# Kernel optimization log

Measured on AMD Instinct MI355X. Metric: run time of the kernel, lower is better.

The kernel has to match this reference:

```python
import jax, jax.numpy as jnp
import numpy as np

N = 50000      # nodes
E = 800000     # edges
HID = 64       # hidden_dim
HEADS = 4
DH = HID // HEADS
PIN = 128      # person_in_dim
DIN = 64       # disease_in_dim
NEXP = 4       # num_experts
K = 2          # topk
L = 2          # n_layers
NEG = 0.2      # gat_neg_slope


def setup_inputs() -> dict:
    key = jax.random.key(0)
    ks = iter(jax.random.split(key, 64))
    nrm = lambda shp, s=0.05: jax.random.normal(next(ks), shp, jnp.float32) * s
    d = {}
    d["features"] = jax.random.normal(next(ks), (N, PIN), jnp.float32)
    d["node_types"] = jax.random.randint(next(ks), (N,), 0, 2)
    d["src"] = jax.random.randint(next(ks), (E,), 0, N)
    d["dst"] = jax.random.randint(next(ks), (E,), 0, N)
    d["W_person"] = nrm((PIN, HID)); d["b_person"] = jnp.zeros((HID,), jnp.float32)
    d["W_disease"] = nrm((DIN, HID)); d["b_disease"] = jnp.zeros((HID,), jnp.float32)
    d["gat_W"] = nrm((L, HID, HID)); d["gat_al"] = nrm((L, HEADS, DH)); d["gat_ar"] = nrm((L, HEADS, DH))
    d["gin_eps"] = jnp.zeros((L,), jnp.float32)
    d["gin_W1"] = nrm((L, HID, HID)); d["gin_b1"] = jnp.zeros((L, HID), jnp.float32)
    d["gin_W2"] = nrm((L, HID, HID)); d["gin_b2"] = jnp.zeros((L, HID), jnp.float32)
    for p in ("gat", "gin"):
        d[p + "_gW"] = nrm((HID, NEXP)); d[p + "_gb"] = jnp.zeros((NEXP,), jnp.float32)
        d[p + "_eW1"] = nrm((NEXP, HID, HID // 2)); d[p + "_eb1"] = jnp.zeros((NEXP, HID // 2), jnp.float32)
        d[p + "_eW2"] = nrm((NEXP, HID // 2, HID)); d[p + "_eb2"] = jnp.zeros((NEXP, HID), jnp.float32)
    d["fg_W1"] = nrm((2 * HID, HID)); d["fg_b1"] = jnp.zeros((HID,), jnp.float32)
    d["fg_W2"] = nrm((HID, HID)); d["fg_b2"] = jnp.zeros((HID,), jnp.float32)
    return d


def _edge_softmax(logits, dst):
    m = jax.ops.segment_max(logits, dst, num_segments=N)
    e = jnp.exp(logits - m[dst])
    s = jax.ops.segment_sum(e, dst, num_segments=N)
    return e / (s[dst] + 1e-9)


def _gat(h, src, dst, gat_W, gat_al, gat_ar):
    for l in range(L):
        hW = (h @ gat_W[l]).reshape(N, HEADS, DH)
        el = (hW * gat_al[l]).sum(-1)                    # [N, HEADS]
        er = (hW * gat_ar[l]).sum(-1)
        lg = jax.nn.leaky_relu(el[src] + er[dst], NEG)   # [E, HEADS]
        a = _edge_softmax(lg, dst)
        out = jax.ops.segment_sum(hW[src] * a[:, :, None], dst, num_segments=N)
        h2 = out.reshape(N, HID) + h                     # residual=True
        h = jax.nn.relu(h2) if l < L - 1 else h2
    return h


def _gin(h, src, dst, gin_eps, gin_W1, gin_b1, gin_W2, gin_b2):
    deg = jax.ops.segment_sum(jnp.ones((E,), jnp.float32), dst, num_segments=N)
    inv = 1.0 / jnp.maximum(deg, 1.0)
    for l in range(L):
        agg = jax.ops.segment_sum(h[src], dst, num_segments=N) * inv[:, None]  # 'mean' aggregator
        x = (1.0 + gin_eps[l]) * h + agg                 # learn_eps=True
        x = jax.nn.relu(x @ gin_W1[l] + gin_b1[l]) @ gin_W2[l] + gin_b2[l]     # 2-layer MLP
        h = jax.nn.relu(x) if l < L - 1 else x
    return h


def _expert(h, gW, gb, eW1, eb1, eW2, eb2):
    probs = jax.nn.softmax(h @ gW + gb, axis=-1)         # [N, NEXP]
    topv, topi = jax.lax.top_k(probs, K)
    topv = topv / topv.sum(-1, keepdims=True)
    hot = jax.nn.one_hot(topi, NEXP, dtype=h.dtype)      # [N, K, NEXP]
    w = (hot * topv[..., None]).sum(1)                   # [N, NEXP] sparse weights
    e1 = jax.nn.relu(jnp.einsum('nd,edh->neh', h, eW1) + eb1)
    e2 = jnp.einsum('neh,ehd->ned', e1, eW2) + eb2       # [N, NEXP, HID]
    out = (e2 * w[:, :, None]).sum(1)
    f = hot.sum(1).mean(0)                               # routed fraction per expert
    P = probs.mean(0)
    aux = NEXP * jnp.sum(f * P)                          # switch-style load balancing
    return out, aux


def reference(features, node_types, src, dst, W_person, b_person, W_disease, b_disease,
              gat_W, gat_al, gat_ar, gin_eps, gin_W1, gin_b1, gin_W2, gin_b2,
              gat_gW, gat_gb, gat_eW1, gat_eb1, gat_eW2, gat_eb2,
              gin_gW, gin_gb, gin_eW1, gin_eb1, gin_eW2, gin_eb2,
              fg_W1, fg_b1, fg_W2, fg_b2):
    # per-type projection + scatter into shared buffer
    hp = features[:, :PIN] @ W_person + b_person
    hd = features[:, :DIN] @ W_disease + b_disease
    h = jnp.where((node_types == 0)[:, None], hp, hd)
    z_gat = _gat(h, src, dst, gat_W, gat_al, gat_ar)
    z_gin = _gin(h, src, dst, gin_eps, gin_W1, gin_b1, gin_W2, gin_b2)
    zg, aux_g = _expert(z_gat, gat_gW, gat_gb, gat_eW1, gat_eb1, gat_eW2, gat_eb2)
    zi, aux_i = _expert(z_gin, gin_gW, gin_gb, gin_eW1, gin_eb1, gin_eW2, gin_eb2)
    z = zi * zg
    u = jnp.concatenate([zg, zi], axis=-1)
    gate = jax.nn.sigmoid(jax.nn.relu(u @ fg_W1 + fg_b1) @ fg_W2 + fg_b2)
    u_prime = gate  # source calls fusion_gate(u) twice -> identical deterministic value
    z = gate * z + (1.0 - gate) * u_prime
    return z, aux_i + aux_g
```

## Files before the change

### kernel.cpp

```cpp
#include <hip/hip_runtime.h>

#define NN 50000
#define EE 800000
#define NEG 0.2f
#define NBLK_SCAN 196
#define NBG 391
#define NBE 196
#define RBLK 782
#define NBKT 98
#define BCAP 9216
#define EPB 2048
#define NBINA 391

typedef __attribute__((ext_vector_type(8))) short s8;
typedef __attribute__((ext_vector_type(4))) float f4;

__device__ __forceinline__ float leaky(float x) { return x > 0.f ? x : NEG * x; }
__device__ __forceinline__ unsigned bf16r(float x) {
    unsigned u = __float_as_uint(x);
    return (u + 0x7fffu + ((u >> 16) & 1u)) >> 16;
}
__device__ __forceinline__ float lo16(unsigned p) { return __uint_as_float(p << 16); }
__device__ __forceinline__ float hi16(unsigned p) { return __uint_as_float(p & 0xffff0000u); }

__device__ __forceinline__ s8 a_from_f32(const float* p) {
    float4 u = *reinterpret_cast<const float4*>(p);
    float4 v = *reinterpret_cast<const float4*>(p + 4);
    s8 r;
    r[0] = (short)bf16r(u.x); r[1] = (short)bf16r(u.y);
    r[2] = (short)bf16r(u.z); r[3] = (short)bf16r(u.w);
    r[4] = (short)bf16r(v.x); r[5] = (short)bf16r(v.y);
    r[6] = (short)bf16r(v.z); r[7] = (short)bf16r(v.w);
    return r;
}

__global__ __launch_bounds__(256) void k_binA(const int* __restrict__ src,
        const int* __restrict__ dst, int* __restrict__ degcnt,
        int* __restrict__ bktcnt, unsigned* __restrict__ bkt) {
    __shared__ int cnt[NBKT];
    __shared__ int base[NBKT];
    for (int i = threadIdx.x; i < NBKT; i += 256) cnt[i] = 0;
    __syncthreads();
    int e0 = blockIdx.x * EPB;
    int d[8], s[8];
    #pragma unroll
    for (int i = 0; i < 8; i++) {
        int e = e0 + i * 256 + threadIdx.x;
        if (e < EE) {
            d[i] = dst[e]; s[i] = src[e];
            atomicAdd(&degcnt[d[i]], 1);
            atomicAdd(&cnt[d[i] >> 9], 1);
        } else d[i] = -1;
    }
    __syncthreads();
    for (int i = threadIdx.x; i < NBKT; i += 256)
        base[i] = atomicAdd(&bktcnt[i], cnt[i]);
    __syncthreads();
    for (int i = threadIdx.x; i < NBKT; i += 256) cnt[i] = 0;
    __syncthreads();
    #pragma unroll
    for (int i = 0; i < 8; i++) {
        if (d[i] >= 0) {
            int b = d[i] >> 9;
            int p = base[b] + atomicAdd(&cnt[b], 1);
            if (p < BCAP)
                bkt[(size_t)b * BCAP + p] = ((unsigned)s[i] << 9) | (unsigned)(d[i] & 511);
        }
    }
}

__global__ void k_scan_a(const int* __restrict__ degcnt, int* __restrict__ bsums) {
    __shared__ int sm[4];
    int i = blockIdx.x * 256 + threadIdx.x;
    int v = (i < NN) ? degcnt[i] : 0;
    #pragma unroll
    for (int o = 1; o < 64; o <<= 1) v += __shfl_xor(v, o, 64);
    if ((threadIdx.x & 63) == 0) sm[threadIdx.x >> 6] = v;
    __syncthreads();
    if (threadIdx.x == 0) bsums[blockIdx.x] = sm[0] + sm[1] + sm[2] + sm[3];
}

__global__ void k_scan_b(const int* __restrict__ bsums, int* __restrict__ bpre) {
    __shared__ int sm[256];
    int t = threadIdx.x;
    sm[t] = (t < NBLK_SCAN) ? bsums[t] : 0;
    __syncthreads();
    for (int off = 1; off < 256; off <<= 1) {
        int u = (t >= off) ? sm[t - off] : 0;
        __syncthreads();
        sm[t] += u;
        __syncthreads();
    }
    if (t < NBLK_SCAN) bpre[t] = (t == 0) ? 0 : sm[t - 1];
}

__global__ void k_scan_c(const int* __restrict__ degcnt, const int* __restrict__ bpre,
                         int* __restrict__ row_start) {
    __shared__ int sm[256];
    int t = threadIdx.x;
    int i = blockIdx.x * 256 + t;
    int v = (i < NN) ? degcnt[i] : 0;
    sm[t] = v;
    __syncthreads();
    for (int off = 1; off < 256; off <<= 1) {
        int u = (t >= off) ? sm[t - off] : 0;
        __syncthreads();
        sm[t] += u;
        __syncthreads();
    }
    int incl = sm[t];
    if (i < NN) row_start[i] = bpre[blockIdx.x] + incl - v;
    if (i == NN - 1) row_start[NN] = bpre[blockIdx.x] + incl;
}

__global__ __launch_bounds__(256) void k_binB_pre(
        const int* __restrict__ row_start, const int* __restrict__ bktcnt,
        const unsigned* __restrict__ bkt, int* __restrict__ csr_src,
        const float* __restrict__ feat, const int* __restrict__ types,
        const float* __restrict__ Wp, const float* __restrict__ bp,
        const float* __restrict__ Wd, const float* __restrict__ bd,
        const float* __restrict__ gW, const float* __restrict__ al,
        const float* __restrict__ ar,
        float* __restrict__ h0f, unsigned* __restrict__ P,
        float* __restrict__ el, float* __restrict__ er) {
    __shared__ unsigned short WpT[64 * 136];
    __shared__ unsigned short WdT[64 * 72];
    __shared__ unsigned short WgT[64 * 72];
    __shared__ unsigned short y0s[4][16 * 72];
    __shared__ int kur[512];
    if (blockIdx.x < NBKT) {
        int b = blockIdx.x;
        int d0 = b << 9;
        for (int i = threadIdx.x; i < 512; i += 256) {
            int d = d0 + i;
            kur[i] = (d < NN) ? row_start[d] : 0;
        }
        __syncthreads();
        int cnt = bktcnt[b]; if (cnt > BCAP) cnt = BCAP;
        for (int i = threadIdx.x; i < cnt; i += 256) {
            unsigned v = bkt[(size_t)b * BCAP + i];
            int p = atomicAdd(&kur[v & 511], 1);
            csr_src[p] = (int)(v >> 9);
        }
        return;
    }
    for (int idx = threadIdx.x; idx < 128 * 64; idx += 256) {
        int k = idx >> 6, n = idx & 63;
        WpT[n * 136 + k] = (unsigned short)bf16r(Wp[idx]);
    }
    for (int idx = threadIdx.x; idx < 64 * 64; idx += 256) {
        int k = idx >> 6, n = idx & 63;
        WdT[n * 72 + k] = (unsigned short)bf16r(Wd[idx]);
        WgT[n * 72 + k] = (unsigned short)bf16r(gW[idx]);
    }
    __syncthreads();
    int wv = threadIdx.x >> 6, lane = threadIdx.x & 63;
    int quad = lane >> 4, l16 = lane & 15;
    int gw2 = (blockIdx.x - NBKT) * 4 + wv;
    int mtEnd = gw2 * 2 + 2; if (mtEnd > 3125) mtEnd = 3125;
    for (int mt = gw2 * 2; mt < mtEnd; mt++) {
        int row0 = mt * 16;
        const float* arow = feat + (size_t)(row0 + l16) * 128;
        f4 accp[4], accd[4];
        #pragma unroll
        for (int t = 0; t < 4; t++) { accp[t] = f4{0.f,0.f,0.f,0.f}; accd[t] = f4{0.f,0.f,0.f,0.f}; }
        #pragma unroll
        for (int ks = 0; ks < 4; ks++) {
            s8 a = a_from_f32(arow + ks * 32 + quad * 8);
            #pragma unroll
            for (int t = 0; t < 4; t++) {
                s8 b = *(const s8*)&WpT[(t * 16 + l16) * 136 + ks * 32 + quad * 8];
                accp[t] = __builtin_amdgcn_mfma_f32_16x16x32_bf16(a, b, accp[t], 0, 0, 0);
                if (ks < 2) {
                    s8 bd_ = *(const s8*)&WdT[(t * 16 + l16) * 72 + ks * 32 + quad * 8];
                    accd[t] = __builtin_amdgcn_mfma_f32_16x16x32_bf16(a, bd_, accd[t], 0, 0, 0);
                }
            }
        }
        int ty[4];
        #pragma unroll
        for (int r = 0; r < 4; r++) ty[r] = types[row0 + quad * 4 + r];
        float vv[4][4];
        #pragma unroll
        for (int t = 0; t < 4; t++) {
            int col = t * 16 + l16;
            float bpv = bp[col], bdv = bd[col];
            #pragma unroll
            for (int r = 0; r < 4; r++) {
                float v = ty[r] ? (accd[t][r] + bdv) : (accp[t][r] + bpv);
                vv[t][r] = v;
                h0f[(size_t)(row0 + quad * 4 + r) * 64 + col] = v;
                y0s[wv][(quad * 4 + r) * 72 + col] = (unsigned short)bf16r(v);
            }
        }
        s8 a0 = *(const s8*)&y0s[wv][l16 * 72 + quad * 8];
        s8 a1 = *(const s8*)&y0s[wv][l16 * 72 + 32 + quad * 8];
        f4 hw[4];
        #pragma unroll
        for (int t = 0; t < 4; t++) {
            hw[t] = f4{0.f,0.f,0.f,0.f};
            s8 b0 = *(const s8*)&WgT[(t * 16 + l16) * 72 + quad * 8];
            hw[t] = __builtin_amdgcn_mfma_f32_16x16x32_bf16(a0, b0, hw[t], 0, 0, 0);
            s8 b1_ = *(const s8*)&WgT[(t * 16 + l16) * 72 + 32 + quad * 8];
            hw[t] = __builtin_amdgcn_mfma_f32_16x16x32_bf16(a1, b1_, hw[t], 0, 0, 0);
        }
        #pragma unroll
        for (int t = 0; t < 4; t++) {
            int col = t * 16 + l16;
            float alv = al[col], arv = ar[col];
            #pragma unroll
            for (int r = 0; r < 4; r++) {
                int row = row0 + quad * 4 + r;
                float h = hw[t][r];
                P[(size_t)row * 64 + col] = bf16r(h) | (bf16r(vv[t][r]) << 16);
                float pl = h * alv, pr = h * arv;
                #pragma unroll
                for (int m = 1; m < 16; m <<= 1) {
                    pl += __shfl_xor(pl, m, 64);
                    pr += __shfl_xor(pr, m, 64);
                }
                if (l16 == 0) {
                    el[(size_t)row * 4 + t] = pl;
                    er[(size_t)row * 4 + t] = pr;
                }
            }
        }
    }
}

template <int RELU>
__global__ void k_edges(const int* __restrict__ rows, const int* __restrict__ csr,
                        const unsigned* __restrict__ Pin,
                        const float* __restrict__ el, const float* __restrict__ er,
                        const float* __restrict__ gat_in, const float* __restrict__ gin_in,
                        const float* __restrict__ eps_p,
                        float* __restrict__ vgf, unsigned short* __restrict__ vgb,
                        unsigned short* __restrict__ xb) {
    __shared__ float ews[4][256];
    int wv = threadIdx.x >> 6, lane = threadIdx.x & 63;
    int n = blockIdx.x * 4 + wv;
    int st = rows[n], dg = rows[n + 1] - st;
    int hd = lane >> 4;
    float4 erv = *reinterpret_cast<const float4*>(er + (size_t)n * 4);
    float accg = 0.f, acci = 0.f, ssum = 0.f;
    for (int base = 0; base < dg; base += 64) {
        int rem = dg - base; if (rem > 64) rem = 64;
        int myi = 0;
        if (lane < rem) {
            myi = csr[st + base + lane];
            float4 lv = *reinterpret_cast<const float4*>(el + (size_t)myi * 4);
            float4 ev;
            ev.x = __expf(leaky(lv.x + erv.x));
            ev.y = __expf(leaky(lv.y + erv.y));
            ev.z = __expf(leaky(lv.z + erv.z));
            ev.w = __expf(leaky(lv.w + erv.w));
            *reinterpret_cast<float4*>(&ews[wv][lane * 4]) = ev;
        }
        int j = 0;
        for (; j + 4 <= rem; j += 4) {
            int s0 = __shfl(myi, j, 64),     s1 = __shfl(myi, j + 1, 64);
            int s2 = __shfl(myi, j + 2, 64), s3 = __shfl(myi, j + 3, 64);
            unsigned p0 = Pin[(size_t)s0 * 64 + lane];
            unsigned p1 = Pin[(size_t)s1 * 64 + lane];
            unsigned p2 = Pin[(size_t)s2 * 64 + lane];
            unsigned p3 = Pin[(size_t)s3 * 64 + lane];
            float a0 = ews[wv][(j + 0) * 4 + hd];
            float a1 = ews[wv][(j + 1) * 4 + hd];
            float a2 = ews[wv][(j + 2) * 4 + hd];
            float a3 = ews[wv][(j + 3) * 4 + hd];
            accg += a0 * lo16(p0) + a1 * lo16(p1) + a2 * lo16(p2) + a3 * lo16(p3);
            acci += hi16(p0) + hi16(p1) + hi16(p2) + hi16(p3);
            ssum += a0 + a1 + a2 + a3;
        }
        for (; j < rem; j++) {
            int s0 = __shfl(myi, j, 64);
            unsigned p0 = Pin[(size_t)s0 * 64 + lane];
            float a0 = ews[wv][j * 4 + hd];
            accg += a0 * lo16(p0); acci += hi16(p0); ssum += a0;
        }
    }
    float vg = accg / (ssum + 1e-9f) + gat_in[(size_t)n * 64 + lane];
    if (RELU) vg = fmaxf(vg, 0.f);
    float invd = 1.0f / fmaxf((float)dg, 1.0f);
    float x = (1.0f + eps_p[0]) * gin_in[(size_t)n * 64 + lane] + acci * invd;
    size_t off = (size_t)n * 64 + lane;
    vgf[off] = vg;
    vgb[off] = (unsigned short)bf16r(vg);
    xb[off] = (unsigned short)bf16r(x);
}

template <int L>
__global__ __launch_bounds__(256) void k_mlp(const unsigned short* __restrict__ Gx,
        const unsigned short* __restrict__ Eb,
        const float* __restrict__ W1, const float* __restrict__ b1,
        const float* __restrict__ W2, const float* __restrict__ b2,
        const float* __restrict__ gatW, const float* __restrict__ al,
        const float* __restrict__ ar,
        unsigned short* __restrict__ Fb, float* __restrict__ Cf,
        unsigned* __restrict__ P, float* __restrict__ el, float* __restrict__ er) {
    __shared__ unsigned short W1T[64 * 72];
    __shared__ unsigned short W2T[64 * 72];
    __shared__ unsigned short WgT[(L == 0) ? 64 * 72 : 64];
    __shared__ unsigned short y1s[4][16 * 72];
    for (int idx = threadIdx.x; idx < 64 * 64; idx += 256) {
        int k = idx >> 6, n = idx & 63;
        W1T[n * 72 + k] = (unsigned short)bf16r(W1[idx]);
        W2T[n * 72 + k] = (unsigned short)bf16r(W2[idx]);
        if (L == 0) WgT[n * 72 + k] = (unsigned short)bf16r(gatW[idx]);
    }
    __syncthreads();
    int wv = threadIdx.x >> 6, lane = threadIdx.x & 63;
    int quad = lane >> 4, l16 = lane & 15;
    int gw = blockIdx.x * 4 + wv;
    int mtEnd = gw * 2 + 2; if (mtEnd > 3125) mtEnd = 3125;
    for (int mt = gw * 2; mt < mtEnd; mt++) {
        int row0 = mt * 16;
        const unsigned short* arow = Gx + (size_t)(row0 + l16) * 64;
        s8 a0 = *(const s8*)(arow + quad * 8);
        s8 a1 = *(const s8*)(arow + 32 + quad * 8);
        f4 acc1[4];
        #pragma unroll
        for (int t = 0; t < 4; t++) {
            acc1[t] = f4{0.f,0.f,0.f,0.f};
            s8 b0 = *(const s8*)&W1T[(t * 16 + l16) * 72 + quad * 8];
            acc1[t] = __builtin_amdgcn_mfma_f32_16x16x32_bf16(a0, b0, acc1[t], 0, 0, 0);
            s8 b1_ = *(const s8*)&W1T[(t * 16 + l16) * 72 + 32 + quad * 8];
            acc1[t] = __builtin_amdgcn_mfma_f32_16x16x32_bf16(a1, b1_, acc1[t], 0, 0, 0);
        }
        #pragma unroll
        for (int t = 0; t < 4; t++) {
            float b1v = b1[t * 16 + l16];
            #pragma unroll
            for (int r = 0; r < 4; r++) {
                float v = fmaxf(acc1[t][r] + b1v, 0.f);
                y1s[wv][(quad * 4 + r) * 72 + t * 16 + l16] = (unsigned short)bf16r(v);
            }
        }
        s8 c0 = *(const s8*)&y1s[wv][l16 * 72 + quad * 8];
        s8 c1 = *(const s8*)&y1s[wv][l16 * 72 + 32 + quad * 8];
        f4 acc2[4];
        #pragma unroll
        for (int t = 0; t < 4; t++) {
            acc2[t] = f4{0.f,0.f,0.f,0.f};
            s8 b0 = *(const s8*)&W2T[(t * 16 + l16) * 72 + quad * 8];
            acc2[t] = __builtin_amdgcn_mfma_f32_16x16x32_bf16(c0, b0, acc2[t], 0, 0, 0);
            s8 b1_ = *(const s8*)&W2T[(t * 16 + l16) * 72 + 32 + quad * 8];
            acc2[t] = __builtin_amdgcn_mfma_f32_16x16x32_bf16(c1, b1_, acc2[t], 0, 0, 0);
        }
        unsigned short vb[4][4];
        #pragma unroll
        for (int t = 0; t < 4; t++) {
            int col = t * 16 + l16;
            float b2v = b2[col];
            #pragma unroll
            for (int r = 0; r < 4; r++) {
                float v = acc2[t][r] + b2v;
                if (L == 0) v = fmaxf(v, 0.f);
                size_t off = (size_t)(row0 + quad * 4 + r) * 64 + col;
                unsigned short vb16 = (unsigned short)bf16r(v);
                vb[t][r] = vb16;
                Fb[off] = vb16;
                Cf[off] = v;
            }
        }
        if (L == 0) {
            const unsigned short* erow = Eb + (size_t)(row0 + l16) * 64;
            s8 e0 = *(const s8*)(erow + quad * 8);
            s8 e1 = *(const s8*)(erow + 32 + quad * 8);
            f4 hw[4];
            #pragma unroll
            for (int t = 0; t < 4; t++) {
                hw[t] = f4{0.f,0.f,0.f,0.f};
                s8 b0 = *(const s8*)&WgT[(t * 16 + l16) * 72 + quad * 8];
                hw[t] = __builtin_amdgcn_mfma_f32_16x16x32_bf16(e0, b0, hw[t], 0, 0, 0);
                s8 b1_ = *(const s8*)&WgT[(t * 16 + l16) * 72 + 32 + quad * 8];
                hw[t] = __builtin_amdgcn_mfma_f32_16x16x32_bf16(e1, b1_, hw[t], 0, 0, 0);
            }
            #pragma unroll
            for (int t = 0; t < 4; t++) {
                int col = t * 16 + l16;
                float alv = al[col], arv = ar[col];
                #pragma unroll
                for (int r = 0; r < 4; r++) {
                    int row = row0 + quad * 4 + r;
                    float h = hw[t][r];
                    P[(size_t)row * 64 + col] = bf16r(h) | ((unsigned)vb[t][r] << 16);
                    float pl = h * alv, pr = h * arv;
                    #pragma unroll
                    for (int m = 1; m < 16; m <<= 1) {
                        pl += __shfl_xor(pl, m, 64);
                        pr += __shfl_xor(pr, m, 64);
                    }
                    if (l16 == 0) {
                        el[(size_t)row * 4 + t] = pl;
                        er[(size_t)row * 4 + t] = pr;
                    }
                }
            }
        }
    }
}

__global__ __launch_bounds__(256) void k_route(const float* __restrict__ zg,
        const float* __restrict__ zi,
        const float* __restrict__ ggW, const float* __restrict__ ggb,
        const float* __restrict__ igW, const float* __restrict__ igb,
        float* __restrict__ wgtg, float* __restrict__ wgti,
        float* __restrict__ stats) {
    __shared__ float zs[64][65];
    __shared__ float gws[256];
    __shared__ float sstat[16];
    if (threadIdx.x < 16) sstat[threadIdx.x] = 0.f;
    int n0 = blockIdx.x * 64;
    int wv = threadIdx.x >> 6, lane = threadIdx.x & 63;
    for (int q = 0; q < 2; q++) {
        const float* Z = q ? zi : zg;
        const float* GW = q ? igW : ggW;
        const float* GB = q ? igb : ggb;
        gws[threadIdx.x] = GW[threadIdx.x];
        #pragma unroll
        for (int r = 0; r < 16; r++) {
            int row = wv * 16 + r;
            int n = n0 + row;
            zs[row][lane] = (n < NN) ? Z[(size_t)n * 64 + lane] : 0.f;
        }
        __syncthreads();
        int node = threadIdx.x >> 2, e = threadIdx.x & 3;
        float lg = GB[e];
        #pragma unroll 8
        for (int k = 0; k < 64; k++) lg += zs[node][k] * gws[k * 4 + e];
        float b = __shfl_xor(lg, 1, 64);
        float c = __shfl_xor(lg, 2, 64);
        float d = __shfl_xor(b, 2, 64);
        float arr[4];
        arr[e] = lg; arr[e ^ 1] = b; arr[e ^ 2] = c; arr[e ^ 3] = d;
        int n = n0 + node;
        if (e == 0 && n < NN) {
            float mx = fmaxf(fmaxf(arr[0], arr[1]), fmaxf(arr[2], arr[3]));
            float ex0 = __expf(arr[0] - mx), ex1 = __expf(arr[1] - mx);
            float ex2 = __expf(arr[2] - mx), ex3 = __expf(arr[3] - mx);
            float inv = 1.0f / (ex0 + ex1 + ex2 + ex3);
            float pr[4] = {ex0 * inv, ex1 * inv, ex2 * inv, ex3 * inv};
            int i1 = 0; float v1 = pr[0];
            #pragma unroll
            for (int t = 1; t < 4; t++) if (pr[t] > v1) { v1 = pr[t]; i1 = t; }
            int i2 = -1; float v2 = -1.f;
            #pragma unroll
            for (int t = 0; t < 4; t++) if (t != i1 && pr[t] > v2) { v2 = pr[t]; i2 = t; }
            float wsum = v1 + v2;
            float wq[4] = {0.f, 0.f, 0.f, 0.f};
            wq[i1] = v1 / wsum; wq[i2] = v2 / wsum;
            float* WD = q ? wgti : wgtg;
            *reinterpret_cast<float4*>(WD + (size_t)n * 4) = float4{wq[0], wq[1], wq[2], wq[3]};
            #pragma unroll
            for (int t = 0; t < 4; t++) atomicAdd(&sstat[q * 8 + t], pr[t]);
            atomicAdd(&sstat[q * 8 + 4 + i1], 1.f);
            atomicAdd(&sstat[q * 8 + 4 + i2], 1.f);
        }
        __syncthreads();
    }
    if (threadIdx.x < 16) atomicAdd(&stats[threadIdx.x], sstat[threadIdx.x]);
}

__global__ __launch_bounds__(256) void k_expert(const unsigned short* __restrict__ Eb,
        const unsigned short* __restrict__ Fb,
        const float* __restrict__ g_eW1, const float* __restrict__ g_eb1,
        const float* __restrict__ g_eW2, const float* __restrict__ g_eb2,
        const float* __restrict__ i_eW1, const float* __restrict__ i_eb1,
        const float* __restrict__ i_eW2, const float* __restrict__ i_eb2,
        const float* __restrict__ wgtg, const float* __restrict__ wgti,
        float* __restrict__ moegf, float* __restrict__ moeif,
        unsigned short* __restrict__ ub) {
    __shared__ unsigned short w1t[4 * 32 * 72];
    __shared__ unsigned short w2t[4 * 64 * 40];
    __shared__ unsigned short y1s[4][16 * 40];
    int p = (blockIdx.x >= NBE) ? 1 : 0;
    int bb = blockIdx.x - p * NBE;
    const unsigned short* Ab = p ? Fb : Eb;
    const float* eW1 = p ? i_eW1 : g_eW1;
    const float* eb1 = p ? i_eb1 : g_eb1;
    const float* eW2 = p ? i_eW2 : g_eW2;
    const float* eb2 = p ? i_eb2 : g_eb2;
    const float* wgt = p ? wgti : wgtg;
    float* moef = p ? moeif : moegf;
    int qoff = p ? 64 : 0;
    for (int g = threadIdx.x; g < 8192; g += 256) {
        int e = g >> 11, rem = g & 2047;
        int k = rem >> 5, n = rem & 31;
        w1t[e * 2304 + n * 72 + k] = (unsigned short)bf16r(eW1[g]);
    }
    for (int g = threadIdx.x; g < 8192; g += 256) {
        int e = g >> 11, rem = g & 2047;
        int k = rem >> 6, n = rem & 63;
        w2t[e * 2560 + n * 40 + k] = (unsigned short)bf16r(eW2[g]);
    }
    __syncthreads();
    int wv = threadIdx.x >> 6, lane = threadIdx.x & 63;
    int quad = lane >> 4, l16 = lane & 15;
    int gw = bb * 4 + wv;
    int mtEnd = gw * 4 + 4; if (mtEnd > 3125) mtEnd = 3125;
    for (int mt = gw * 4; mt < mtEnd; mt++) {
        int row0 = mt * 16;
        const unsigned short* arow = Ab + (size_t)(row0 + l16) * 64;
        s8 a0 = *(const s8*)(arow + quad * 8);
        s8 a1 = *(const s8*)(arow + 32 + quad * 8);
        f4 outacc[4];
        #pragma unroll
        for (int t = 0; t < 4; t++) outacc[t] = f4{0.f,0.f,0.f,0.f};
        for (int e = 0; e < 4; e++) {
            f4 acc1[2];
            #pragma unroll
            for (int t = 0; t < 2; t++) {
                acc1[t] = f4{0.f,0.f,0.f,0.f};
                s8 b0 = *(const s8*)&w1t[e * 2304 + (t * 16 + l16) * 72 + quad * 8];
                acc1[t] = __builtin_amdgcn_mfma_f32_16x16x32_bf16(a0, b0, acc1[t], 0, 0, 0);
                s8 b1_ = *(const s8*)&w1t[e * 2304 + (t * 16 + l16) * 72 + 32 + quad * 8];
                acc1[t] = __builtin_amdgcn_mfma_f32_16x16x32_bf16(a1, b1_, acc1[t], 0, 0, 0);
            }
            #pragma unroll
            for (int t = 0; t < 2; t++) {
                float b1v = eb1[e * 32 + t * 16 + l16];
                #pragma unroll
                for (int r = 0; r < 4; r++) {
                    float v = fmaxf(acc1[t][r] + b1v, 0.f);
                    y1s[wv][(quad * 4 + r) * 40 + t * 16 + l16] = (unsigned short)bf16r(v);
                }
            }
            s8 a2 = *(const s8*)&y1s[wv][l16 * 40 + quad * 8];
            f4 acc2[4];
            #pragma unroll
            for (int t = 0; t < 4; t++) {
                acc2[t] = f4{0.f,0.f,0.f,0.f};
                s8 b2_ = *(const s8*)&w2t[e * 2560 + (t * 16 + l16) * 40 + quad * 8];
                acc2[t] = __builtin_amdgcn_mfma_f32_16x16x32_bf16(a2, b2_, acc2[t], 0, 0, 0);
            }
            #pragma unroll
            for (int t = 0; t < 4; t++) {
                float b2v = eb2[e * 64 + t * 16 + l16];
                #pragma unroll
                for (int r = 0; r < 4; r++) {
                    float we = wgt[(size_t)(row0 + quad * 4 + r) * 4 + e];
                    outacc[t][r] += we * (acc2[t][r] + b2v);
                }
            }
        }
        #pragma unroll
        for (int t = 0; t < 4; t++) {
            int col = t * 16 + l16;
            #pragma unroll
            for (int r = 0; r < 4; r++) {
                int row = row0 + quad * 4 + r;
                float v = outacc[t][r];
                moef[(size_t)row * 64 + col] = v;
                ub[(size_t)row * 128 + qoff + col] = (unsigned short)bf16r(v);
            }
        }
    }
}

__global__ __launch_bounds__(256) void k_fusion(const unsigned short* __restrict__ ubuf,
        const float* __restrict__ W1, const float* __restrict__ b1,
        const float* __restrict__ W2, const float* __restrict__ b2,
        const float* __restrict__ moegf, const float* __restrict__ moeif,
        float* __restrict__ out, const float* __restrict__ stats) {
    __shared__ unsigned short W1T[64 * 136];
    __shared__ unsigned short W2T[64 * 72];
    __shared__ unsigned short y1s[4][16 * 72];
    for (int idx = threadIdx.x; idx < 128 * 64; idx += 256) {
        int k = idx >> 6, n = idx & 63;
        W1T[n * 136 + k] = (unsigned short)bf16r(W1[idx]);
    }
    for (int idx = threadIdx.x; idx < 64 * 64; idx += 256) {
        int k = idx >> 6, n = idx & 63;
        W2T[n * 72 + k] = (unsigned short)bf16r(W2[idx]);
    }
    __syncthreads();
    int wv = threadIdx.x >> 6, lane = threadIdx.x & 63;
    int quad = lane >> 4, l16 = lane & 15;
    int gw = blockIdx.x * 4 + wv;
    int mtEnd = gw * 2 + 2; if (mtEnd > 3125) mtEnd = 3125;
    for (int mt = gw * 2; mt < mtEnd; mt++) {
        int row0 = mt * 16;
        const unsigned short* arow = ubuf + (size_t)(row0 + l16) * 128;
        f4 acc1[4];
        #pragma unroll
        for (int t = 0; t < 4; t++) acc1[t] = f4{0.f,0.f,0.f,0.f};
        #pragma unroll
        for (int ks = 0; ks < 4; ks++) {
            s8 a = *(const s8*)(arow + ks * 32 + quad * 8);
            #pragma unroll
            for (int t = 0; t < 4; t++) {
                s8 b = *(const s8*)&W1T[(t * 16 + l16) * 136 + ks * 32 + quad * 8];
                acc1[t] = __builtin_amdgcn_mfma_f32_16x16x32_bf16(a, b, acc1[t], 0, 0, 0);
            }
        }
        #pragma unroll
        for (int t = 0; t < 4; t++) {
            float b1v = b1[t * 16 + l16];
            #pragma unroll
            for (int r = 0; r < 4; r++) {
                float v = fmaxf(acc1[t][r] + b1v, 0.f);
                y1s[wv][(quad * 4 + r) * 72 + t * 16 + l16] = (unsigned short)bf16r(v);
            }
        }
        f4 acc2[4];
        #pragma unroll
        for (int t = 0; t < 4; t++) acc2[t] = f4{0.f,0.f,0.f,0.f};
        #pragma unroll
        for (int ks = 0; ks < 2; ks++) {
            s8 a = *(const s8*)&y1s[wv][l16 * 72 + ks * 32 + quad * 8];
            #pragma unroll
            for (int t = 0; t < 4; t++) {
                s8 b = *(const s8*)&W2T[(t * 16 + l16) * 72 + ks * 32 + quad * 8];
                acc2[t] = __builtin_amdgcn_mfma_f32_16x16x32_bf16(a, b, acc2[t], 0, 0, 0);
            }
        }
        #pragma unroll
        for (int t = 0; t < 4; t++) {
            int col = t * 16 + l16;
            float b2v = b2[col];
            #pragma unroll
            for (int r = 0; r < 4; r++) {
                int row = row0 + quad * 4 + r;
                float g = 1.0f / (1.0f + __expf(-(acc2[t][r] + b2v)));
                float zgv = moegf[(size_t)row * 64 + col];
                float ziv = moeif[(size_t)row * 64 + col];
                out[(size_t)row * 64 + col] = g * zgv * ziv + (1.0f - g) * g;
            }
        }
    }
    if (blockIdx.x == 0 && threadIdx.x < 64) {
        int t = threadIdx.x;
        float s = (t < 16) ? stats[t] : 0.f;
        float aux = 0.f;
        for (int q = 0; q < 2; q++) {
            float a = 0.f;
            for (int e = 0; e < 4; e++) {
                float pr = __shfl(s, q * 8 + e, 64);
                float f  = __shfl(s, q * 8 + 4 + e, 64);
                a += (f / (float)NN) * (pr / (float)NN);
            }
            aux += 4.0f * a;
        }
        if (t == 0) out[(size_t)NN * 64] = aux;
    }
}

extern "C" void kernel_launch(void* const* d_in, const int* in_sizes, int n_in,
                              void* d_out, int out_size, void* d_ws, size_t ws_size,
                              hipStream_t stream) {
    (void)in_sizes; (void)n_in; (void)out_size; (void)ws_size;
    const float* features  = (const float*)d_in[0];
    const int*   node_types= (const int*)d_in[1];
    const int*   src       = (const int*)d_in[2];
    const int*   dst       = (const int*)d_in[3];
    const float* W_person  = (const float*)d_in[4];
    const float* b_person  = (const float*)d_in[5];
    const float* W_disease = (const float*)d_in[6];
    const float* b_disease = (const float*)d_in[7];
    const float* gat_W     = (const float*)d_in[8];
    const float* gat_al    = (const float*)d_in[9];
    const float* gat_ar    = (const float*)d_in[10];
    const float* gin_eps   = (const float*)d_in[11];
    const float* gin_W1    = (const float*)d_in[12];
    const float* gin_b1    = (const float*)d_in[13];
    const float* gin_W2    = (const float*)d_in[14];
    const float* gin_b2    = (const float*)d_in[15];
    const float* gat_gW    = (const float*)d_in[16];
    const float* gat_gb    = (const float*)d_in[17];
    const float* gat_eW1   = (const float*)d_in[18];
    const float* gat_eb1   = (const float*)d_in[19];
    const float* gat_eW2   = (const float*)d_in[20];
    const float* gat_eb2   = (const float*)d_in[21];
    const float* gin_gW    = (const float*)d_in[22];
    const float* gin_gb    = (const float*)d_in[23];
    const float* gin_eW1   = (const float*)d_in[24];
    const float* gin_eb1   = (const float*)d_in[25];
    const float* gin_eW2   = (const float*)d_in[26];
    const float* gin_eb2   = (const float*)d_in[27];
    const float* fg_W1     = (const float*)d_in[28];
    const float* fg_b1     = (const float*)d_in[29];
    const float* fg_W2     = (const float*)d_in[30];
    const float* fg_b2     = (const float*)d_in[31];
    float* out = (float*)d_out;

    float* ws = (float*)d_ws;
    size_t o = 0;
    float* A = ws + o; o += (size_t)NN * 64;
    float* B = ws + o; o += (size_t)NN * 64;
    float* C = ws + o; o += (size_t)NN * 64;
    unsigned short* E  = (unsigned short*)(ws + o); o += (size_t)NN * 32;
    unsigned short* F  = (unsigned short*)(ws + o); o += (size_t)NN * 32;
    unsigned short* G  = (unsigned short*)(ws + o); o += (size_t)NN * 32;
    unsigned* P = (unsigned*)(ws + o); o += (size_t)NN * 64;
    float* el = ws + o; o += (size_t)NN * 4;
    float* er = ws + o; o += (size_t)NN * 4;
    float* wgtg = ws + o; o += (size_t)NN * 4;
    float* wgti = ws + o; o += (size_t)NN * 4;
    int* degcnt    = (int*)(ws + o); o += NN;
    int* bktcnt    = (int*)(ws + o); o += NBKT;
    float* stats   = ws + o; o += 16;
    int* row_start = (int*)(ws + o); o += NN + 4;
    int* bsums     = (int*)(ws + o); o += 256;
    int* bpre      = (int*)(ws + o); o += 256;
    int* csr_src   = (int*)(ws + o); o += EE;
    unsigned* bkt  = (unsigned*)(ws + o); o += (size_t)NBKT * BCAP;

    unsigned short* ub = (unsigned short*)A;

    const int NB_node = NN / 4;

    hipMemsetAsync(degcnt, 0, sizeof(int) * (NN + NBKT) + sizeof(float) * 16, stream);

    k_binA<<<NBINA, 256, 0, stream>>>(src, dst, degcnt, bktcnt, bkt);
    k_scan_a<<<NBLK_SCAN, 256, 0, stream>>>(degcnt, bsums);
    k_scan_b<<<1, 256, 0, stream>>>(bsums, bpre);
    k_scan_c<<<NBLK_SCAN, 256, 0, stream>>>(degcnt, bpre, row_start);

    k_binB_pre<<<NBKT + NBG, 256, 0, stream>>>(row_start, bktcnt, bkt, csr_src,
                                               features, node_types, W_person, b_person,
                                               W_disease, b_disease, gat_W, gat_al, gat_ar,
                                               A, P, el, er);

    k_edges<1><<<NB_node, 256, 0, stream>>>(row_start, csr_src, P, el, er, A, A,
                                            gin_eps, B, E, G);
    k_mlp<0><<<NBG, 256, 0, stream>>>(G, E, gin_W1, gin_b1, gin_W2, gin_b2,
                                      gat_W + 4096, gat_al + 64, gat_ar + 64,
                                      F, C, P, el, er);

    k_edges<0><<<NB_node, 256, 0, stream>>>(row_start, csr_src, P, el, er, B, C,
                                            gin_eps + 1, B, E, G);
    k_mlp<1><<<NBG, 256, 0, stream>>>(G, nullptr, gin_W1 + 4096, gin_b1 + 64,
                                      gin_W2 + 4096, gin_b2 + 64,
                                      nullptr, nullptr, nullptr,
                                      F, C, nullptr, nullptr, nullptr);

    k_route<<<RBLK, 256, 0, stream>>>(B, C, gat_gW, gat_gb, gin_gW, gin_gb,
                                      wgtg, wgti, stats);
    k_expert<<<NBE * 2, 256, 0, stream>>>(E, F,
                                          gat_eW1, gat_eb1, gat_eW2, gat_eb2,
                                          gin_eW1, gin_eb1, gin_eW2, gin_eb2,
                                          wgtg, wgti, B, C, ub);

    k_fusion<<<NBG, 256, 0, stream>>>(ub, fg_W1, fg_b1, fg_W2, fg_b2, B, C, out, stats);
}
```

Baseline: 367.7 us.

## Use per-block segment binning for CSR build and fuse MoE routing into MLP

Edge binning now does a block-local counting sort into shared memory and writes contiguous per-block segments with per-bucket offsets and counts. This replaces global atomics on bucket counters and removes the fixed bucket capacity. The CSR fill stage then walks all segments for its bucket. The separate routing kernel is folded into the second GIN MLP kernel, which computes gate logits, top-2 weights and load stats from in-register outputs, so the fp32 z_gin store and the routing re-read are skipped. The price is many short per-segment loops in the CSR scatter with poor lane use, plus extra register pressure and shuffles in the MLP kernel.

Result: slower. 401.3 us (+9.1%).

```diff
diff --git a/kernel.cpp b/kernel.cpp
--- a/kernel.cpp
+++ b/kernel.cpp
@@ -6,11 +6,9 @@
 #define NBLK_SCAN 196
 #define NBG 391
 #define NBE 196
-#define RBLK 782
 #define NBKT 98
-#define BCAP 9216
 #define EPB 2048
-#define NBINA 391
+#define NSEG 391
 
 typedef __attribute__((ext_vector_type(8))) short s8;
 typedef __attribute__((ext_vector_type(4))) float f4;
@@ -36,37 +34,48 @@
 
 __global__ __launch_bounds__(256) void k_binA(const int* __restrict__ src,
         const int* __restrict__ dst, int* __restrict__ degcnt,
-        int* __restrict__ bktcnt, unsigned* __restrict__ bkt) {
+        int* __restrict__ seg_off, int* __restrict__ seg_cnt,
+        unsigned* __restrict__ gseg) {
     __shared__ int cnt[NBKT];
-    __shared__ int base[NBKT];
+    __shared__ int pre[128];
+    __shared__ unsigned sbuf[EPB];
     for (int i = threadIdx.x; i < NBKT; i += 256) cnt[i] = 0;
     __syncthreads();
     int e0 = blockIdx.x * EPB;
-    int d[8], s[8];
+    int nE = EE - e0; if (nE > EPB) nE = EPB;
+    int b[8]; unsigned val[8]; int rk[8];
     #pragma unroll
     for (int i = 0; i < 8; i++) {
-        int e = e0 + i * 256 + threadIdx.x;
-        if (e < EE) {
-            d[i] = dst[e]; s[i] = src[e];
-            atomicAdd(&degcnt[d[i]], 1);
-            atomicAdd(&cnt[d[i] >> 9], 1);
-        } else d[i] = -1;
-    }
-    __syncthreads();
-    for (int i = threadIdx.x; i < NBKT; i += 256)
-        base[i] = atomicAdd(&bktcnt[i], cnt[i]);
-    __syncthreads();
-    for (int i = threadIdx.x; i < NBKT; i += 256) cnt[i] = 0;
-    __syncthreads();
+        int li = i * 256 + threadIdx.x;
+        if (li < nE) {
+            int e = e0 + li;
+            int d = dst[e], s = src[e];
+            atomicAdd(&degcnt[d], 1);
+            b[i] = d >> 9;
+            val[i] = ((unsigned)s << 9) | (unsigned)(d & 511);
+            rk[i] = atomicAdd(&cnt[b[i]], 1);
+        } else b[i] = -1;
+    }
+    __syncthreads();
+    if (threadIdx.x < 128) pre[threadIdx.x] = (threadIdx.x < NBKT) ? cnt[threadIdx.x] : 0;
+    __syncthreads();
+    for (int off = 1; off < 128; off <<= 1) {
+        int v = 0;
+        if (threadIdx.x < 128 && threadIdx.x >= off) v = pre[threadIdx.x - off];
+        __syncthreads();
+        if (threadIdx.x < 128) pre[threadIdx.x] += v;
+        __syncthreads();
+    }
     #pragma unroll
-    for (int i = 0; i < 8; i++) {
-        if (d[i] >= 0) {
-            int b = d[i] >> 9;
-            int p = base[b] + atomicAdd(&cnt[b], 1);
-            if (p < BCAP)
-                bkt[(size_t)b * BCAP + p] = ((unsigned)s[i] << 9) | (unsigned)(d[i] & 511);
-        }
-    }
+    for (int i = 0; i < 8; i++)
+        if (b[i] >= 0) sbuf[pre[b[i]] - cnt[b[i]] + rk[i]] = val[i];
+    if (threadIdx.x < NBKT) {
+        seg_off[blockIdx.x * NBKT + threadIdx.x] = pre[threadIdx.x] - cnt[threadIdx.x];
+        seg_cnt[blockIdx.x * NBKT + threadIdx.x] = cnt[threadIdx.x];
+    }
+    __syncthreads();
+    for (int i = threadIdx.x; i < nE; i += 256)
+        gseg[(size_t)blockIdx.x * EPB + i] = sbuf[i];
 }
 
 __global__ void k_scan_a(const int* __restrict__ degcnt, int* __restrict__ bsums) {
@@ -114,8 +123,9 @@
 }
 
 __global__ __launch_bounds__(256) void k_binB_pre(
-        const int* __restrict__ row_start, const int* __restrict__ bktcnt,
-        const unsigned* __restrict__ bkt, int* __restrict__ csr_src,
+        const int* __restrict__ row_start, const int* __restrict__ seg_off,
+        const int* __restrict__ seg_cnt, const unsigned* __restrict__ gseg,
+        int* __restrict__ csr_src,
         const float* __restrict__ feat, const int* __restrict__ types,
         const float* __restrict__ Wp, const float* __restrict__ bp,
         const float* __restrict__ Wd, const float* __restrict__ bd,
@@ -136,11 +146,15 @@
             kur[i] = (d < NN) ? row_start[d] : 0;
         }
         __syncthreads();
-        int cnt = bktcnt[b]; if (cnt > BCAP) cnt = BCAP;
-        for (int i = threadIdx.x; i < cnt; i += 256) {
-            unsigned v = bkt[(size_t)b * BCAP + i];
-            int p = atomicAdd(&kur[v & 511], 1);
-            csr_src[p] = (int)(v >> 9);
+        int wv = threadIdx.x >> 6, lane = threadIdx.x & 63;
+        for (int seg = wv; seg < NSEG; seg += 4) {
+            int off = seg_off[seg * NBKT + b];
+            int c = seg_cnt[seg * NBKT + b];
+            for (int i = lane; i < c; i += 64) {
+                unsigned v = gseg[(size_t)seg * EPB + off + i];
+                int p = atomicAdd(&kur[v & 511], 1);
+                csr_src[p] = (int)(v >> 9);
+            }
         }
         return;
     }
@@ -297,11 +311,18 @@
         const float* __restrict__ gatW, const float* __restrict__ al,
         const float* __restrict__ ar,
         unsigned short* __restrict__ Fb, float* __restrict__ Cf,
-        unsigned* __restrict__ P, float* __restrict__ el, float* __restrict__ er) {
+        unsigned* __restrict__ P, float* __restrict__ el, float* __restrict__ er,
+        const float* __restrict__ Zg, const float* __restrict__ ggW,
+        const float* __restrict__ ggb, const float* __restrict__ igW,
+        const float* __restrict__ igb,
+        float* __restrict__ wgtg, float* __restrict__ wgti,
+        float* __restrict__ stats) {
     __shared__ unsigned short W1T[64 * 72];
     __shared__ unsigned short W2T[64 * 72];
     __shared__ unsigned short WgT[(L == 0) ? 64 * 72 : 64];
     __shared__ unsigned short y1s[4][16 * 72];
+    __shared__ float sstat[16];
+    if (L == 1 && threadIdx.x < 16) sstat[threadIdx.x] = 0.f;
     for (int idx = threadIdx.x; idx < 64 * 64; idx += 256) {
         int k = idx >> 6, n = idx & 63;
         W1T[n * 72 + k] = (unsigned short)bf16r(W1[idx]);
@@ -313,6 +334,8 @@
     int quad = lane >> 4, l16 = lane & 15;
     int gw = blockIdx.x * 4 + wv;
     int mtEnd = gw * 2 + 2; if (mtEnd > 3125) mtEnd = 3125;
+    float sp[2][4] = {{0,0,0,0},{0,0,0,0}};
+    float sh[2][4] = {{0,0,0,0},{0,0,0,0}};
     for (int mt = gw * 2; mt < mtEnd; mt++) {
         int row0 = mt * 16;
         const unsigned short* arow = Gx + (size_t)(row0 + l16) * 64;
@@ -348,6 +371,7 @@
             acc2[t] = __builtin_amdgcn_mfma_f32_16x16x32_bf16(c1, b1_, acc2[t], 0, 0, 0);
         }
         unsigned short vb[4][4];
+        float vout[4][4];
         #pragma unroll
         for (int t = 0; t < 4; t++) {
             int col = t * 16 + l16;
@@ -359,8 +383,9 @@
                 size_t off = (size_t)(row0 + quad * 4 + r) * 64 + col;
                 unsigned short vb16 = (unsigned short)bf16r(v);
                 vb[t][r] = vb16;
+                vout[t][r] = v;
                 Fb[off] = vb16;
-                Cf[off] = v;
+                if (L == 0) Cf[off] = v;
             }
         }
         if (L == 0) {
@@ -397,69 +422,76 @@
                     }
                 }
             }
-        }
-    }
-}
-
-__global__ __launch_bounds__(256) void k_route(const float* __restrict__ zg,
-        const float* __restrict__ zi,
-        const float* __restrict__ ggW, const float* __restrict__ ggb,
-        const float* __restrict__ igW, const float* __restrict__ igb,
-        float* __restrict__ wgtg, float* __restrict__ wgti,
-        float* __restrict__ stats) {
-    __shared__ float zs[64][65];
-    __shared__ float gws[256];
-    __shared__ float sstat[16];
-    if (threadIdx.x < 16) sstat[threadIdx.x] = 0.f;
-    int n0 = blockIdx.x * 64;
-    int wv = threadIdx.x >> 6, lane = threadIdx.x & 63;
-    for (int q = 0; q < 2; q++) {
-        const float* Z = q ? zi : zg;
-        const float* GW = q ? igW : ggW;
-        const float* GB = q ? igb : ggb;
-        gws[threadIdx.x] = GW[threadIdx.x];
-        #pragma unroll
-        for (int r = 0; r < 16; r++) {
-            int row = wv * 16 + r;
-            int n = n0 + row;
-            zs[row][lane] = (n < NN) ? Z[(size_t)n * 64 + lane] : 0.f;
-        }
-        __syncthreads();
-        int node = threadIdx.x >> 2, e = threadIdx.x & 3;
-        float lg = GB[e];
-        #pragma unroll 8
-        for (int k = 0; k < 64; k++) lg += zs[node][k] * gws[k * 4 + e];
-        float b = __shfl_xor(lg, 1, 64);
-        float c = __shfl_xor(lg, 2, 64);
-        float d = __shfl_xor(b, 2, 64);
-        float arr[4];
-        arr[e] = lg; arr[e ^ 1] = b; arr[e ^ 2] = c; arr[e ^ 3] = d;
-        int n = n0 + node;
-        if (e == 0 && n < NN) {
-            float mx = fmaxf(fmaxf(arr[0], arr[1]), fmaxf(arr[2], arr[3]));
-            float ex0 = __expf(arr[0] - mx), ex1 = __expf(arr[1] - mx);
-            float ex2 = __expf(arr[2] - mx), ex3 = __expf(arr[3] - mx);
-            float inv = 1.0f / (ex0 + ex1 + ex2 + ex3);
-            float pr[4] = {ex0 * inv, ex1 * inv, ex2 * inv, ex3 * inv};
-            int i1 = 0; float v1 = pr[0];
-            #pragma unroll
-            for (int t = 1; t < 4; t++) if (pr[t] > v1) { v1 = pr[t]; i1 = t; }
-            int i2 = -1; float v2 = -1.f;
-            #pragma unroll
-            for (int t = 0; t < 4; t++) if (t != i1 && pr[t] > v2) { v2 = pr[t]; i2 = t; }
-            float wsum = v1 + v2;
-            float wq[4] = {0.f, 0.f, 0.f, 0.f};
-            wq[i1] = v1 / wsum; wq[i2] = v2 / wsum;
-            float* WD = q ? wgti : wgtg;
-            *reinterpret_cast<float4*>(WD + (size_t)n * 4) = float4{wq[0], wq[1], wq[2], wq[3]};
-            #pragma unroll
-            for (int t = 0; t < 4; t++) atomicAdd(&sstat[q * 8 + t], pr[t]);
-            atomicAdd(&sstat[q * 8 + 4 + i1], 1.f);
-            atomicAdd(&sstat[q * 8 + 4 + i2], 1.f);
-        }
-        __syncthreads();
-    }
-    if (threadIdx.x < 16) atomicAdd(&stats[threadIdx.x], sstat[threadIdx.x]);
+        } else {
+            #pragma unroll
+            for (int r = 0; r < 4; r++) {
+                int row = row0 + quad * 4 + r;
+                float pg[4] = {0,0,0,0}, pi[4] = {0,0,0,0};
+                #pragma unroll
+                for (int t = 0; t < 4; t++) {
+                    int col = t * 16 + l16;
+                    float zgv = Zg[(size_t)row * 64 + col];
+                    float ziv = vout[t][r];
+                    #pragma unroll
+                    for (int e = 0; e < 4; e++) {
+                        pg[e] += zgv * ggW[col * 4 + e];
+                        pi[e] += ziv * igW[col * 4 + e];
+                    }
+                }
+                #pragma unroll
+                for (int m = 1; m < 16; m <<= 1) {
+                    #pragma unroll
+                    for (int e = 0; e < 4; e++) {
+                        pg[e] += __shfl_xor(pg[e], m, 64);
+                        pi[e] += __shfl_xor(pi[e], m, 64);
+                    }
+                }
+                if (l16 == 0) {
+                    #pragma unroll
+                    for (int q = 0; q < 2; q++) {
+                        float lg0 = (q ? pi[0] + igb[0] : pg[0] + ggb[0]);
+                        float lg1 = (q ? pi[1] + igb[1] : pg[1] + ggb[1]);
+                        float lg2 = (q ? pi[2] + igb[2] : pg[2] + ggb[2]);
+                        float lg3 = (q ? pi[3] + igb[3] : pg[3] + ggb[3]);
+                        float mx = fmaxf(fmaxf(lg0, lg1), fmaxf(lg2, lg3));
+                        float ex0 = __expf(lg0 - mx), ex1 = __expf(lg1 - mx);
+                        float ex2 = __expf(lg2 - mx), ex3 = __expf(lg3 - mx);
+                        float inv = 1.0f / (ex0 + ex1 + ex2 + ex3);
+                        float pr4[4] = {ex0 * inv, ex1 * inv, ex2 * inv, ex3 * inv};
+                        int i1 = 0; float v1 = pr4[0];
+                        #pragma unroll
+                        for (int t = 1; t < 4; t++) if (pr4[t] > v1) { v1 = pr4[t]; i1 = t; }
+                        int i2 = -1; float v2 = -1.f;
+                        #pragma unroll
+                        for (int t = 0; t < 4; t++) if (t != i1 && pr4[t] > v2) { v2 = pr4[t]; i2 = t; }
+                        float wsum = v1 + v2;
+                        float wq[4] = {0.f, 0.f, 0.f, 0.f};
+                        wq[i1] = v1 / wsum; wq[i2] = v2 / wsum;
+                        float* WD = q ? wgti : wgtg;
+                        *reinterpret_cast<float4*>(WD + (size_t)row * 4) =
+                            float4{wq[0], wq[1], wq[2], wq[3]};
+                        #pragma unroll
+                        for (int t = 0; t < 4; t++) sp[q][t] += pr4[t];
+                        sh[q][i1] += 1.f; sh[q][i2] += 1.f;
+                    }
+                }
+            }
+        }
+    }
+    if (L == 1) {
+        __syncthreads();
+        if (l16 == 0) {
+            #pragma unroll
+            for (int q = 0; q < 2; q++)
+                #pragma unroll
+                for (int e = 0; e < 4; e++) {
+                    atomicAdd(&sstat[q * 8 + e], sp[q][e]);
+                    atomicAdd(&sstat[q * 8 + 4 + e], sh[q][e]);
+                }
+        }
+        __syncthreads();
+        if (threadIdx.x < 16) atomicAdd(&stats[threadIdx.x], sstat[threadIdx.x]);
+    }
 }
 
 __global__ __launch_bounds__(256) void k_expert(const unsigned short* __restrict__ Eb,
@@ -698,26 +730,27 @@
     float* wgtg = ws + o; o += (size_t)NN * 4;
     float* wgti = ws + o; o += (size_t)NN * 4;
     int* degcnt    = (int*)(ws + o); o += NN;
-    int* bktcnt    = (int*)(ws + o); o += NBKT;
     float* stats   = ws + o; o += 16;
     int* row_start = (int*)(ws + o); o += NN + 4;
     int* bsums     = (int*)(ws + o); o += 256;
     int* bpre      = (int*)(ws + o); o += 256;
     int* csr_src   = (int*)(ws + o); o += EE;
-    unsigned* bkt  = (unsigned*)(ws + o); o += (size_t)NBKT * BCAP;
+    int* seg_off   = (int*)(ws + o); o += NSEG * NBKT + 64;
+    int* seg_cnt   = (int*)(ws + o); o += NSEG * NBKT + 64;
+    unsigned* gseg = (unsigned*)(ws + o); o += (size_t)NSEG * EPB;
 
     unsigned short* ub = (unsigned short*)A;
 
     const int NB_node = NN / 4;
 
-    hipMemsetAsync(degcnt, 0, sizeof(int) * (NN + NBKT) + sizeof(float) * 16, stream);
-
-    k_binA<<<NBINA, 256, 0, stream>>>(src, dst, degcnt, bktcnt, bkt);
+    hipMemsetAsync(degcnt, 0, sizeof(int) * NN + sizeof(float) * 16, stream);
+
+    k_binA<<<NSEG, 256, 0, stream>>>(src, dst, degcnt, seg_off, seg_cnt, gseg);
     k_scan_a<<<NBLK_SCAN, 256, 0, stream>>>(degcnt, bsums);
     k_scan_b<<<1, 256, 0, stream>>>(bsums, bpre);
     k_scan_c<<<NBLK_SCAN, 256, 0, stream>>>(degcnt, bpre, row_start);
 
-    k_binB_pre<<<NBKT + NBG, 256, 0, stream>>>(row_start, bktcnt, bkt, csr_src,
+    k_binB_pre<<<NBKT + NBG, 256, 0, stream>>>(row_start, seg_off, seg_cnt, gseg, csr_src,
                                                features, node_types, W_person, b_person,
                                                W_disease, b_disease, gat_W, gat_al, gat_ar,
                                                A, P, el, er);
@@ -726,17 +759,19 @@
                                             gin_eps, B, E, G);
     k_mlp<0><<<NBG, 256, 0, stream>>>(G, E, gin_W1, gin_b1, gin_W2, gin_b2,
                                       gat_W + 4096, gat_al + 64, gat_ar + 64,
-                                      F, C, P, el, er);
+                                      F, C, P, el, er,
+                                      nullptr, nullptr, nullptr, nullptr, nullptr,
+                                      nullptr, nullptr, nullptr);
 
     k_edges<0><<<NB_node, 256, 0, stream>>>(row_start, csr_src, P, el, er, B, C,
                                             gin_eps + 1, B, E, G);
     k_mlp<1><<<NBG, 256, 0, stream>>>(G, nullptr, gin_W1 + 4096, gin_b1 + 64,
                                       gin_W2 + 4096, gin_b2 + 64,
                                       nullptr, nullptr, nullptr,
-                                      F, C, nullptr, nullptr, nullptr);
-
-    k_route<<<RBLK, 256, 0, stream>>>(B, C, gat_gW, gat_gb, gin_gW, gin_gb,
+                                      F, nullptr, nullptr, nullptr, nullptr,
+                                      B, gat_gW, gat_gb, gin_gW, gin_gb,
                                       wgtg, wgti, stats);
+
     k_expert<<<NBE * 2, 256, 0, stream>>>(E, F,
                                           gat_eW1, gat_eb1, gat_eW2, gat_eb2,
                                           gin_eW1, gin_eb1, gin_eW2, gin_eb2,
```
